# Optimization experiments

Hardware: AMD Instinct MI355X
Metric: run time of the kernel (lower is better)

## Reference

```python
import jax, jax.numpy as jnp
import numpy as np

N, T, CIN = 40000, 32, 8
VW = 64          # back_voxelwise_channels
P = 16           # v2b_maxvoxels (voxels stacked per BEV cell)
BEV_H, BEV_W = 496, 432
EPS = 1e-5


def _bn(key, shape):
    # returns stacked (gamma, beta, running_mean, running_var) along axis -2
    k1, k2, k3 = jax.random.split(key, 3)
    g = 1.0 + 0.1 * jax.random.normal(k1, shape, jnp.float32)
    b = 0.1 * jax.random.normal(k2, shape, jnp.float32)
    m = 0.1 * jax.random.normal(k3, shape, jnp.float32)
    v = jnp.ones(shape, jnp.float32)
    return jnp.stack([g, b, m, v], axis=-2)


def setup_inputs() -> dict:
    key = jax.random.key(0)
    ks = jax.random.split(key, 20)
    features = jax.random.normal(ks[0], (N, T, CIN), jnp.float32)
    cy = jax.random.randint(ks[1], (N, 1), 0, BEV_H)
    cx = jax.random.randint(ks[2], (N, 1), 0, BEV_W)
    coors = jnp.concatenate([cy, cx], axis=1).astype(jnp.int32)
    num_voxels = jax.random.randint(ks[3], (N,), 1, T + 1).astype(jnp.int32)

    def w(k, o, i):
        return jax.random.normal(k, (o, i), jnp.float32) / float(np.sqrt(i))

    return dict(
        features=features, coors=coors, num_voxels=num_voxels,
        vfe1_W=w(ks[4], 8, CIN), vfe1_bn=_bn(ks[5], (8,)),
        vfe2_W=w(ks[6], 32, 16), vfe2_bn=_bn(ks[7], (32,)),
        vfe3_W=w(ks[8], 64, 64), vfe3_bn=_bn(ks[9], (64,)),
        vfe4_W=w(ks[10], 64, 64), vfe4_bn=_bn(ks[11], (64,)),
        bfe1_W=jax.random.normal(ks[12], (16, P, P), jnp.float32) / float(np.sqrt(P)),
        bfe1_bn=_bn(ks[13], (16, P)),
        bfe2_W=jax.random.normal(ks[14], (16, 2, P), jnp.float32) / float(np.sqrt(P)),
        bfe2_bn=_bn(ks[15], (16, 2)),
        bfe3_W=w(ks[16], 128, 128), bfe3_bn=_bn(ks[17], (128,)),
    )


def _forward(features, vfe1_W, vfe1_bn, vfe2_W, vfe2_bn, vfe3_W, vfe3_bn,
             vfe4_W, vfe4_bn, bfe1_W, bfe1_bn, bfe2_W, bfe2_bn, bfe3_W, bfe3_bn,
             coors, num_voxels):
    n, t = features.shape[0], features.shape[1]
    f32 = features.dtype
    mask = (jnp.arange(t)[None, :] < num_voxels[:, None]).astype(f32)[..., None]  # [N,T,1]

    def fe(x, W, bn):  # Linear (no bias) + BatchNorm1d (eval) + Mish
        g, b, m, v = bn
        y = x @ W.T
        y = (y - m) * jax.lax.rsqrt(v + EPS) * g + b
        return y * jnp.tanh(jax.nn.softplus(y))

    def vfe(x, W, bn):  # pointwise FE, max-pool over points, concat
        p = fe(x, W, bn)
        agg = jnp.max(p, axis=1, keepdims=True)
        return jnp.concatenate([p, jnp.broadcast_to(agg, p.shape)], axis=2)

    x1 = vfe(features, vfe1_W, vfe1_bn)           # [N,T,16]
    x2 = vfe(x1, vfe2_W, vfe2_bn) * mask          # [N,T,64]
    x3 = fe(x2, vfe3_W, vfe3_bn)
    x4 = fe(x3, vfe4_W, vfe4_bn) * mask + x2
    voxelwise = jnp.max(x4, axis=1)               # [N,64]

    # ---- voxel2bev: group voxels by BEV cell, stack up to P per cell ----
    cell = coors[:, 0] * BEV_W + coors[:, 1]                         # [N]
    ucell, inv = jnp.unique(cell, return_inverse=True, size=n, fill_value=BEV_H * BEV_W)
    order = jnp.argsort(inv)                                          # stable
    inv_sorted = inv[order]
    pos_sorted = jnp.arange(n) - jnp.searchsorted(inv_sorted, inv_sorted, side='left')
    slot = jnp.zeros(n, jnp.int32).at[order].set(pos_sorted.astype(jnp.int32))
    row = jnp.where(slot < P, inv, n)                                 # overflow -> dropped
    bevs = jnp.zeros((n, P, VW), f32).at[row, jnp.minimum(slot, P - 1)].set(
        voxelwise, mode='drop')                                       # [N,P,64]
    counts = jax.ops.segment_sum(jnp.ones(n, jnp.int32), inv, num_segments=n)
    numv = jnp.minimum(counts, P)
    bevcoors = jnp.stack([ucell // BEV_W, ucell % BEV_W], axis=1)     # [N,2]

    # ---- 16 grouped FE stacks over the slot dimension ----
    x0 = bevs.transpose(0, 2, 1).reshape(n, 16, 4, P)                 # [N,16,4,P]
    m2 = (jnp.arange(P)[None, :] < numv[:, None]).astype(f32)[:, None, None, :]
    y = jnp.einsum('ngip,gqp->ngiq', x0, bfe1_W)                      # [N,16,4,P]
    g1, b1, m1, v1 = (bfe1_bn[None, :, i, None, :] for i in range(4))
    y = (y - m1) * jax.lax.rsqrt(v1 + EPS) * g1 + b1
    y = y * jnp.tanh(jax.nn.softplus(y)) * m2
    z = jnp.einsum('ngip,gcp->ngic', y, bfe2_W)                       # [N,16,4,2]
    g2, b2, m2b, v2 = (bfe2_bn[None, :, i, None, :] for i in range(4))
    z = (z - m2b) * jax.lax.rsqrt(v2 + EPS) * g2 + b2
    z = z * jnp.tanh(jax.nn.softplus(z))
    # torch cat along dim=-1 then view -> layout [N, 4, 16, 2] flattened
    x17 = z.transpose(0, 2, 1, 3).reshape(n, 128)
    x18 = fe(x17, bfe3_W, bfe3_bn)
    x19 = fe(x18, bfe3_W, bfe3_bn)   # original applies bfe3 twice (bfe4 unused)

    bevmap = jnp.zeros((BEV_H, BEV_W, 128), f32).at[
        bevcoors[:, 0], bevcoors[:, 1]].set(x19, mode='drop')
    return bevmap.transpose(2, 1, 0)                                  # [128, W, H]


def reference(features, coors, num_voxels, vfe1_W, vfe1_bn, vfe2_W, vfe2_bn,
              vfe3_W, vfe3_bn, vfe4_W, vfe4_bn, bfe1_W, bfe1_bn, bfe2_W, bfe2_bn,
              bfe3_W, bfe3_bn):
    return _forward(features, vfe1_W, vfe1_bn, vfe2_W, vfe2_bn, vfe3_W, vfe3_bn,
                    vfe4_W, vfe4_bn, bfe1_W, bfe1_bn, bfe2_W, bfe2_bn,
                    bfe3_W, bfe3_bn, coors, num_voxels)
```

## Files before the change

kernel.cpp:

```cpp
#include <hip/hip_runtime.h>

#define BEVW 432
#define BEVH 496
#define NCELL (BEVW*BEVH)
#define NVOX  40000
#define EPSB  1e-5f

typedef float f32x2 __attribute__((ext_vector_type(2)));
typedef float f32x4 __attribute__((ext_vector_type(4)));
typedef unsigned int u32x4 __attribute__((ext_vector_type(4)));
typedef short bf16x8 __attribute__((ext_vector_type(8)));

#define REP8_0(M)  M(0) M(1) M(2) M(3) M(4) M(5) M(6) M(7)
#define REP8_8(M)  M(8) M(9) M(10) M(11) M(12) M(13) M(14) M(15)
#define REP8_16(M) M(16) M(17) M(18) M(19) M(20) M(21) M(22) M(23)
#define REP8_24(M) M(24) M(25) M(26) M(27) M(28) M(29) M(30) M(31)
#define REP16_0(M)  REP8_0(M)  REP8_8(M)
#define REP32_0(M) REP16_0(M) REP8_16(M) REP8_24(M)


__device__ __forceinline__ float mishf(float y) {
    float e = __expf(fminf(y, 40.f));
    float n = e * (e + 2.f);
    return y * n * __builtin_amdgcn_rcpf(n + 2.f);
}

template <int CTRL>
__device__ __forceinline__ float dppmaxf(float a) {
    int p = __builtin_amdgcn_update_dpp(0, __float_as_int(a), CTRL, 0xF, 0xF, true);
    return fmaxf(a, __int_as_float(p));
}
#define WMAX32(a) { \
    a = dppmaxf<0xB1>(a); \
    a = dppmaxf<0x4E>(a); \
    a = dppmaxf<0x141>(a); \
    a = dppmaxf<0x140>(a); \
    a = fmaxf(a, __int_as_float(__builtin_amdgcn_ds_swizzle(__float_as_int(a), 0x401F))); }

__device__ __forceinline__ bf16x8 mkbf8(uint a, uint b, uint c, uint d) {
    u32x4 t = {a, b, c, d};
    return __builtin_bit_cast(bf16x8, t);
}

__device__ __forceinline__ uint splitbf(float x) {
    uint rh = __float_as_uint(x) & 0xFFFF0000u;
    float lof = x - __uint_as_float(rh);
    uint ul = __float_as_uint(lof);
    uint rl = (ul + 0x7FFFu + ((ul >> 16) & 1u)) >> 16;
    return (rh >> 16) | (rl << 16);
}

__global__ __launch_bounds__(256) void setup_kernel(
    const float* __restrict__ vbn1, const float* __restrict__ vbn2,
    const float* __restrict__ vbn3, const float* __restrict__ vbn4,
    const float* __restrict__ bbn1, const float* __restrict__ bbn2,
    const float* __restrict__ bbn3, const float* __restrict__ W4,
    const float* __restrict__ W3g,
    float* __restrict__ fold, ushort* __restrict__ w4fh, ushort* __restrict__ w4fl,
    ushort* __restrict__ w3fh, ushort* __restrict__ w3fl)
{
    int tid = threadIdx.x;
    if (tid < 8)  { float s = vbn1[tid]/sqrtf(vbn1[24+tid]+EPSB);  fold[tid]      = s; fold[8+tid]   = vbn1[8+tid]  - vbn1[16+tid]*s; }
    if (tid < 32) { float s = vbn2[tid]/sqrtf(vbn2[96+tid]+EPSB);  fold[16+tid]   = s; fold[48+tid]  = vbn2[32+tid] - vbn2[64+tid]*s; }
    if (tid < 64) { float s = vbn3[tid]/sqrtf(vbn3[192+tid]+EPSB); fold[80+tid]   = s; fold[144+tid] = vbn3[64+tid] - vbn3[128+tid]*s; }
    if (tid < 64) { float s = vbn4[tid]/sqrtf(vbn4[192+tid]+EPSB); fold[208+tid]  = s; fold[272+tid] = vbn4[64+tid] - vbn4[128+tid]*s; }
    if (tid < 128){ float s = bbn3[tid]/sqrtf(bbn3[384+tid]+EPSB); fold[336+tid]  = s; fold[464+tid] = bbn3[128+tid]- bbn3[256+tid]*s; }
    { int g = tid >> 4, q = tid & 15;
      const float* b = bbn1 + g*64;
      float s = b[q]/sqrtf(b[48+q]+EPSB);
      fold[592+tid] = s; fold[848+tid] = b[16+q] - b[32+q]*s; }
    if (tid < 32) { int g = tid >> 1, c = tid & 1;
      const float* b = bbn2 + g*8;
      float s = b[c]/sqrtf(b[6+c]+EPSB);
      fold[1104+tid] = s; fold[1136+tid] = b[2+c] - b[4+c]*s; }

    for (int i = tid; i < 4096; i += 256) {
        int j = i & 7, ln = (i >> 3) & 63, nt = (i >> 9) & 3, kc = i >> 11;
        int n = (ln & 15) + nt*16;
        int k = kc*32 + (ln >> 4)*8 + j;
        {
            float val = W4[n*64 + k];
            uint rh = __float_as_uint(val) & 0xFFFF0000u;
            float lof = val - __uint_as_float(rh);
            uint ul = __float_as_uint(lof);
            uint rl = (ul + 0x7FFFu + ((ul >> 16) & 1u)) >> 16;
            w4fh[i] = (ushort)(rh >> 16);
            w4fl[i] = (ushort)rl;
        }
        {
            float val = W3g[n*64 + k];
            uint rh = __float_as_uint(val) & 0xFFFF0000u;
            float lof = val - __uint_as_float(rh);
            uint ul = __float_as_uint(lof);
            uint rl = (ul + 0x7FFFu + ((ul >> 16) & 1u)) >> 16;
            w3fh[i] = (ushort)(rh >> 16);
            w3fl[i] = (ushort)rl;
        }
    }
}

#define PAIRS(M) M(0,0,1) M(1,2,3) M(2,4,5) M(3,6,7) M(4,8,9) M(5,10,11) \
  M(6,12,13) M(7,14,15) M(8,16,17) M(9,18,19) M(10,20,21) M(11,22,23) \
  M(12,24,25) M(13,26,27) M(14,28,29) M(15,30,31)

#define MF3(D, AH, AL, BH, BL) \
    D = __builtin_amdgcn_mfma_f32_16x16x32_bf16(AL, BH, D, 0, 0, 0); \
    D = __builtin_amdgcn_mfma_f32_16x16x32_bf16(AH, BL, D, 0, 0, 0); \
    D = __builtin_amdgcn_mfma_f32_16x16x32_bf16(AH, BH, D, 0, 0, 0);

#define DOMTX(SRCP, BHP, BLP, mt, D0, D1, D2, D3) { \
    const uint* ap_ = (SRCP) + ((lane & 15) + 16*(mt))*33 + quad*8; \
    uint u0 = ap_[0], u1 = ap_[1], u2 = ap_[2], u3 = ap_[3]; \
    uint u4 = ap_[4], u5 = ap_[5], u6 = ap_[6], u7 = ap_[7]; \
    bf16x8 Ah = mkbf8(__builtin_amdgcn_perm(u1,u0,0x05040100), __builtin_amdgcn_perm(u3,u2,0x05040100), \
                      __builtin_amdgcn_perm(u5,u4,0x05040100), __builtin_amdgcn_perm(u7,u6,0x05040100)); \
    bf16x8 Al = mkbf8(__builtin_amdgcn_perm(u1,u0,0x07060302), __builtin_amdgcn_perm(u3,u2,0x07060302), \
                      __builtin_amdgcn_perm(u5,u4,0x07060302), __builtin_amdgcn_perm(u7,u6,0x07060302)); \
    { uint4 h = (BHP)[0];   uint4 l = (BLP)[0];   bf16x8 Bh = mkbf8(h.x,h.y,h.z,h.w), Bl = mkbf8(l.x,l.y,l.z,l.w); MF3(D0, Ah, Al, Bh, Bl) } \
    { uint4 h = (BHP)[64];  uint4 l = (BLP)[64];  bf16x8 Bh = mkbf8(h.x,h.y,h.z,h.w), Bl = mkbf8(l.x,l.y,l.z,l.w); MF3(D1, Ah, Al, Bh, Bl) } \
    { uint4 h = (BHP)[128]; uint4 l = (BLP)[128]; bf16x8 Bh = mkbf8(h.x,h.y,h.z,h.w), Bl = mkbf8(l.x,l.y,l.z,l.w); MF3(D2, Ah, Al, Bh, Bl) } \
    { uint4 h = (BHP)[192]; uint4 l = (BLP)[192]; bf16x8 Bh = mkbf8(h.x,h.y,h.z,h.w), Bl = mkbf8(l.x,l.y,l.z,l.w); MF3(D3, Ah, Al, Bh, Bl) } }

__global__ __launch_bounds__(64, 3) void vfe_kernel(
    const float* __restrict__ feat, const int* __restrict__ coors,
    const int* __restrict__ nvx,
    const float* __restrict__ W1, const float* __restrict__ W2,
    const ushort* __restrict__ w3fh, const ushort* __restrict__ w3fl,
    const ushort* __restrict__ w4fh, const ushort* __restrict__ w4fl,
    const float* __restrict__ fold,
    float* __restrict__ voxelwise, int* __restrict__ cnt,
    int* __restrict__ list, int* __restrict__ nact, int* __restrict__ act)
{
    __shared__ char ldsbuf[17152];
    int tid = threadIdx.x;
    int lane = tid;
    int quad = lane >> 4;
    int v = blockIdx.x * 2 + (tid >> 5);
    int vA = blockIdx.x * 2;
    int t = tid & 31;
    uint*  x2s  = (uint*)ldsbuf;
    float* aggL = (float*)(ldsbuf + 16896);

    const float* fp = feat + (v*32 + t)*8;
    float4 fa = *(const float4*)fp;
    float4 fb = *(const float4*)(fp+4);
    int numv = nvx[v];
    float maskf = (t < numv) ? 1.f : 0.f;

#define D1(o) float x1_##o; float m1_##o;
    REP8_0(D1)
#undef D1
#define FE1(o) { const float* w = W1 + (o)*8; \
    float ya = fa.x*w[0] + fa.y*w[1]; float yb = fa.z*w[2] + fa.w*w[3]; \
    float yc = fb.x*w[4] + fb.y*w[5]; float yd = fb.z*w[6] + fb.w*w[7]; \
    float yy = ((ya+yb)+(yc+yd)) * fold[(o)] + fold[8+(o)]; \
    x1_##o = mishf(yy); }
    REP8_0(FE1)
#undef FE1
#define P1(o) { float a = x1_##o; WMAX32(a); m1_##o = a; }
    REP8_0(P1)
#undef P1

    f32x2 x1p_0 = {x1_0,x1_1}, x1p_1 = {x1_2,x1_3}, x1p_2 = {x1_4,x1_5}, x1p_3 = {x1_6,x1_7};
    f32x2 m1p_0 = {m1_0,m1_1}, m1p_1 = {m1_2,m1_3}, m1p_2 = {m1_4,m1_5}, m1p_3 = {m1_6,m1_7};

#define D2(o) float x2_##o; float agg_##o;
    REP32_0(D2)
#undef D2
#define FE2(o) { const f32x2* wp = (const f32x2*)(W2 + (o)*16); \
    f32x2 sa = x1p_0*wp[0]; sa += x1p_1*wp[1]; \
    f32x2 sb = x1p_2*wp[2]; sb += x1p_3*wp[3]; \
    f32x2 sc = m1p_0*wp[4]; sc += m1p_1*wp[5]; \
    f32x2 sd = m1p_2*wp[6]; sd += m1p_3*wp[7]; \
    sa += sb; sc += sd; sa += sc; \
    float yy = (sa.x + sa.y) * fold[16+(o)] + fold[48+(o)]; \
    x2_##o = mishf(yy); }
    REP32_0(FE2)
#undef FE2
#define P2(o) { float a = x2_##o; WMAX32(a); agg_##o = a; }
    REP32_0(P2)
#undef P2

#define PX(i,a,b) f32x2 x2p_##i = {x2_##a, x2_##b}; f32x2 aggp_##i = {agg_##a, agg_##b};
    PAIRS(PX)
#undef PX

    f32x2 maskp = {maskf, maskf};
#define MSK(i) x2p_##i *= maskp; aggp_##i *= maskp;
    REP16_0(MSK)
#undef MSK

    if (t == 0) {
        float* ag = aggL + (lane >> 5)*32;
#define AGW(i) ag[2*(i)] = aggp_##i.x; ag[2*(i)+1] = aggp_##i.y;
        REP16_0(AGW)
#undef AGW
    }

    int nA = __shfl(numv, 0);
    int nB = __shfl(numv, 32);

#define X2W(i) { \
    x2s[lane*33 + 2*(i)]          = splitbf(x2p_##i.x); \
    x2s[lane*33 + 2*(i)+1]        = splitbf(x2p_##i.y); \
    x2s[2112 + lane*33 + 2*(i)]   = splitbf(aggp_##i.x); \
    x2s[2112 + lane*33 + 2*(i)+1] = splitbf(aggp_##i.y); }
    REP16_0(X2W)
#undef X2W

#define E_DECL(i) f32x4 e_##i = {0.f,0.f,0.f,0.f};
    REP16_0(E_DECL)
#undef E_DECL
    {
        const uint4* bh3 = (const uint4*)w3fh + lane;
        const uint4* bl3 = (const uint4*)w3fl + lane;
        DOMTX(x2s, bh3, bl3, 0, e_0, e_1, e_2, e_3)
        DOMTX(x2s, bh3, bl3, 1, e_4, e_5, e_6, e_7)
        DOMTX(x2s, bh3, bl3, 2, e_8, e_9, e_10, e_11)
        DOMTX(x2s, bh3, bl3, 3, e_12, e_13, e_14, e_15)
    }
    {
        const uint4* bh3 = (const uint4*)w3fh + 256 + lane;
        const uint4* bl3 = (const uint4*)w3fl + 256 + lane;
        const uint* sp = x2s + 2112;
        DOMTX(sp, bh3, bl3, 0, e_0, e_1, e_2, e_3)
        DOMTX(sp, bh3, bl3, 1, e_4, e_5, e_6, e_7)
        DOMTX(sp, bh3, bl3, 2, e_8, e_9, e_10, e_11)
        DOMTX(sp, bh3, bl3, 3, e_12, e_13, e_14, e_15)
    }

    int c0 = lane & 15;
    uint* x3st = x2s + 2112;
#define DD(i) f32x4 d_##i = {0.f,0.f,0.f,0.f};
    REP16_0(DD)
#undef DD

#define POST(TI, mt, nt) { \
    float s_ = fold[80 + c0 + 16*(nt)], tb_ = fold[144 + c0 + 16*(nt)]; \
    int col_ = c0 + 16*((nt)&1); \
    int rowb_ = quad*4 + 16*(mt); \
    x3st[(rowb_+0)*33 + col_] = splitbf(mishf(e_##TI.x * s_ + tb_)); \
    x3st[(rowb_+1)*33 + col_] = splitbf(mishf(e_##TI.y * s_ + tb_)); \
    x3st[(rowb_+2)*33 + col_] = splitbf(mishf(e_##TI.z * s_ + tb_)); \
    x3st[(rowb_+3)*33 + col_] = splitbf(mishf(e_##TI.w * s_ + tb_)); }

    {
        POST(0,0,0)  POST(1,0,1)
        POST(4,1,0)  POST(5,1,1)
        POST(8,2,0)  POST(9,2,1)
        POST(12,3,0) POST(13,3,1)
        const uint4* bh4 = (const uint4*)w4fh + lane;
        const uint4* bl4 = (const uint4*)w4fl + lane;
        DOMTX(x3st, bh4, bl4, 0, d_0, d_1, d_2, d_3)
        DOMTX(x3st, bh4, bl4, 1, d_4, d_5, d_6, d_7)
        DOMTX(x3st, bh4, bl4, 2, d_8, d_9, d_10, d_11)
        DOMTX(x3st, bh4, bl4, 3, d_12, d_13, d_14, d_15)
    }
    {
        POST(2,0,2)  POST(3,0,3)
        POST(6,1,2)  POST(7,1,3)
        POST(10,2,2) POST(11,2,3)
        POST(14,3,2) POST(15,3,3)
        const uint4* bh4 = (const uint4*)w4fh + 256 + lane;
        const uint4* bl4 = (const uint4*)w4fl + 256 + lane;
        DOMTX(x3st, bh4, bl4, 0, d_0, d_1, d_2, d_3)
        DOMTX(x3st, bh4, bl4, 1, d_4, d_5, d_6, d_7)
        DOMTX(x3st, bh4, bl4, 2, d_8, d_9, d_10, d_11)
        DOMTX(x3st, bh4, bl4, 3, d_12, d_13, d_14, d_15)
    }
#undef POST

    float s0f = fold[208+c0],    t0f = fold[272+c0];
    float s1f = fold[208+16+c0], t1f = fold[272+16+c0];
    float s2f = fold[208+32+c0], t2f = fold[272+32+c0];
    float s3f = fold[208+48+c0], t3f = fold[272+48+c0];
    float rA2 = aggL[c0],      rA3 = aggL[16+c0];
    float rB2 = aggL[32+c0],   rB3 = aggL[48+c0];
    float pA0=-3.4e38f, pA1=-3.4e38f, pA2=-3.4e38f, pA3=-3.4e38f;
    float pB0=-3.4e38f, pB1=-3.4e38f, pB2=-3.4e38f, pB3=-3.4e38f;

#define RECON(u) (__uint_as_float((u)<<16) + __uint_as_float((u) & 0xFFFF0000u))
#define FTP(D, mt, nt, SS, TT, PV) { \
    int nv = ((mt) >> 1) ? nB : nA; \
    int rf = quad*4 + 16*(mt); \
    int rt = quad*4 + 16*((mt)&1); \
    int cb = c0 + 16*(nt); \
    float m0=(rt+0<nv)?1.f:0.f, m1=(rt+1<nv)?1.f:0.f, m2=(rt+2<nv)?1.f:0.f, m3=(rt+3<nv)?1.f:0.f; \
    uint ua_ = x2s[(rf+0)*33 + cb], ub_ = x2s[(rf+1)*33 + cb]; \
    uint uc_ = x2s[(rf+2)*33 + cb], ud_ = x2s[(rf+3)*33 + cb]; \
    float y0 = mishf(D.x*SS + TT)*m0 + RECON(ua_); \
    float y1 = mishf(D.y*SS + TT)*m1 + RECON(ub_); \
    float y2 = mishf(D.z*SS + TT)*m2 + RECON(uc_); \
    float y3 = mishf(D.w*SS + TT)*m3 + RECON(ud_); \
    PV = fmaxf(PV, fmaxf(fmaxf(y0,y1), fmaxf(y2,y3))); }

#define FTA(D, mt, nt, SS, TT, AG, PV) { \
    int nv = ((mt) >> 1) ? nB : nA; \
    int rt = quad*4 + 16*((mt)&1); \
    float m0=(rt+0<nv)?1.f:0.f, m1=(rt+1<nv)?1.f:0.f, m2=(rt+2<nv)?1.f:0.f, m3=(rt+3<nv)?1.f:0.f; \
    float y0 = (mishf(D.x*SS + TT) + AG)*m0; \
    float y1 = (mishf(D.y*SS + TT) + AG)*m1; \
    float y2 = (mishf(D.z*SS + TT) + AG)*m2; \
    float y3 = (mishf(D.w*SS + TT) + AG)*m3; \
    PV = fmaxf(PV, fmaxf(fmaxf(y0,y1), fmaxf(y2,y3))); }

    FTP(d_0, 0, 0, s0f, t0f, pA0)  FTP(d_1, 0, 1, s1f, t1f, pA1)
    FTA(d_2, 0, 2, s2f, t2f, rA2, pA2)  FTA(d_3, 0, 3, s3f, t3f, rA3, pA3)
    FTP(d_4, 1, 0, s0f, t0f, pA0)  FTP(d_5, 1, 1, s1f, t1f, pA1)
    FTA(d_6, 1, 2, s2f, t2f, rA2, pA2)  FTA(d_7, 1, 3, s3f, t3f, rA3, pA3)
    FTP(d_8, 2, 0, s0f, t0f, pB0)  FTP(d_9, 2, 1, s1f, t1f, pB1)
    FTA(d_10, 2, 2, s2f, t2f, rB2, pB2)  FTA(d_11, 2, 3, s3f, t3f, rB3, pB3)
    FTP(d_12, 3, 0, s0f, t0f, pB0)  FTP(d_13, 3, 1, s1f, t1f, pB1)
    FTA(d_14, 3, 2, s2f, t2f, rB2, pB2)  FTA(d_15, 3, 3, s3f, t3f, rB3, pB3)
#undef FTP
#undef FTA
#undef RECON

#define RED(p) p = fmaxf(p, __shfl_xor(p, 16)); p = fmaxf(p, __shfl_xor(p, 32));
    RED(pA0) RED(pA1) RED(pA2) RED(pA3) RED(pB0) RED(pB1) RED(pB2) RED(pB3)
#undef RED

    if (quad == 0) {
        float* vwA = voxelwise + vA*64;
        vwA[c0] = pA0; vwA[c0+16] = pA1; vwA[c0+32] = pA2; vwA[c0+48] = pA3;
        float* vwB = voxelwise + (vA+1)*64;
        vwB[c0] = pB0; vwB[c0+16] = pB1; vwB[c0+32] = pB2; vwB[c0+48] = pB3;
    }

    if (t == 0) {
        int cell = coors[v*2] * BEVW + coors[v*2+1];
        int pos = atomicAdd(&cnt[cell], 1);
        if (pos < 16) list[cell*16 + pos] = v;
        if (pos == 0) { int k = atomicAdd(nact, 1); act[k] = cell; }
    }
}

__global__ __launch_bounds__(256) void bfe_front(
    const int* __restrict__ nact, const int* __restrict__ act,
    const int* __restrict__ cnt, const int* __restrict__ list,
    const float* __restrict__ voxelwise,
    const float* __restrict__ W1g, const float* __restrict__ W2g,
    const float* __restrict__ fold, float* __restrict__ x17g,
    int* __restrict__ idx)
{
    int n_act = *nact;
    int aidx = blockIdx.x * 4 + (threadIdx.x >> 6);
    if (aidx >= n_act) return;

    int lane = threadIdx.x & 63;
    int g = lane >> 2, ii = lane & 3;
    int cell = act[aidx];
    int numv = min(cnt[cell], 16);
    if (lane == 0) idx[cell] = aidx + 1;

    int myidx = (lane < numv) ? list[cell*16 + lane] : (0x40000000 + lane);
    int rank = 0;
    for (int j = 0; j < numv; j++) { int vj = __shfl(myidx, j); rank += (vj < myidx) ? 1 : 0; }
    if (lane >= numv) rank = lane;
    int sorted = __builtin_amdgcn_ds_permute(rank << 2, myidx);

#define YD(q) float y_##q = 0.f;
    REP16_0(YD)
#undef YD
    for (int p = 0; p < numv; p++) {
        int sv = __shfl(sorted, p);
        float val = voxelwise[sv*64 + lane];
        const float* w = W1g + g*256 + p;
#define BF1(q) y_##q += val * w[(q)*16];
        REP16_0(BF1)
#undef BF1
    }
#define BN1(q) { float yy = y_##q * fold[592 + g*16 + (q)] + fold[848 + g*16 + (q)]; \
    yy = mishf(yy); y_##q = ((q) < numv) ? yy : 0.f; }
    REP16_0(BN1)
#undef BN1

    float z0 = 0.f, z1 = 0.f;
#define BF2(p) z0 += y_##p * W2g[g*32 + (p)]; z1 += y_##p * W2g[g*32 + 16 + (p)];
    REP16_0(BF2)
#undef BF2
    z0 = mishf(z0 * fold[1104 + g*2 + 0] + fold[1136 + g*2 + 0]);
    z1 = mishf(z1 * fold[1104 + g*2 + 1] + fold[1136 + g*2 + 1]);

    int k0 = ii*32 + g*2;
    *(float2*)(x17g + aidx*128 + k0) = make_float2(z0, z1);
}

__global__ __launch_bounds__(512, 4) void bfe3_fused(
    const int* __restrict__ nactp,
    const float* __restrict__ W3, const float* __restrict__ fold,
    float* __restrict__ x17g)
{
    __shared__ float XL[64*128];
    int tid = threadIdx.x;
    int n_act = *nactp;
    int cb = blockIdx.x * 64;

    for (int i = tid; i < 64*32; i += 512) {
        int c = i >> 5, kc = i & 31;
        float4 val = (cb + c < n_act) ? ((const float4*)x17g)[(size_t)(cb+c)*32 + kc]
                                      : make_float4(0.f,0.f,0.f,0.f);
        ((float4*)XL)[c*32 + (kc ^ (c & 31))] = val;
    }
    __syncthreads();

    int wv = __builtin_amdgcn_readfirstlane(tid >> 6);
    int c  = tid & 63;
    int ob = wv * 16;
    int cswz = c & 31;
    const float4* xrow = (const float4*)XL + c*32;
    const float4* W4p = (const float4*)W3;

#define DECLB(q) f32x2 ap_##q = {0.f, 0.f};
#define ACCB(q) { const f32x2* wp_ = (const f32x2*)(W4p + (ob+(q))*32 + kc); \
    ap_##q += xv01 * wp_[0]; ap_##q += xv23 * wp_[1]; }
#define ACTB(q) float a_##q; { float yy = (ap_##q.x + ap_##q.y) * fold[336+ob+(q)] + fold[464+ob+(q)]; a_##q = mishf(yy); }
    {
        REP16_0(DECLB)
        for (int kc = 0; kc < 32; kc++) {
            float4 xv = xrow[kc ^ cswz];
            f32x2 xv01 = {xv.x, xv.y}, xv23 = {xv.z, xv.w};
            REP16_0(ACCB)
        }
        REP16_0(ACTB)
        __syncthreads();
        ((float4*)XL)[c*32 + ((wv*4 + 0) ^ cswz)] = make_float4(a_0,  a_1,  a_2,  a_3);
        ((float4*)XL)[c*32 + ((wv*4 + 1) ^ cswz)] = make_float4(a_4,  a_5,  a_6,  a_7);
        ((float4*)XL)[c*32 + ((wv*4 + 2) ^ cswz)] = make_float4(a_8,  a_9,  a_10, a_11);
        ((float4*)XL)[c*32 + ((wv*4 + 3) ^ cswz)] = make_float4(a_12, a_13, a_14, a_15);
    }
    __syncthreads();

    {
        const float4* yrow = (const float4*)XL + c*32;
        REP16_0(DECLB)
        for (int kc = 0; kc < 32; kc++) {
            float4 xv = yrow[kc ^ cswz];
            f32x2 xv01 = {xv.x, xv.y}, xv23 = {xv.z, xv.w};
            REP16_0(ACCB)
        }
        REP16_0(ACTB)
        float4* dst = (float4*)(x17g + (size_t)(cb + c)*128 + ob);
        dst[0] = make_float4(a_0,  a_1,  a_2,  a_3);
        dst[1] = make_float4(a_4,  a_5,  a_6,  a_7);
        dst[2] = make_float4(a_8,  a_9,  a_10, a_11);
        dst[3] = make_float4(a_12, a_13, a_14, a_15);
    }
#undef DECLB
#undef ACCB
#undef ACTB
}

__global__ __launch_bounds__(512, 2) void bev_write(
    const int* __restrict__ idx, const float* __restrict__ x19c,
    float* __restrict__ out)
{
    __shared__ float XT[128*65];
    int bid = blockIdx.x;
    int cx = bid % BEVW;
    int cy0 = (bid / BEVW) << 6;
    int tid = threadIdx.x;

    int cell_l = tid >> 3;
    int chq = (tid & 7) << 4;
    int cy = cy0 + cell_l;
    float4 v0 = make_float4(0.f,0.f,0.f,0.f), v1 = v0, v2 = v0, v3 = v0;
    if (cy < BEVH) {
        int ai = idx[cy*BEVW + cx] - 1;
        if (ai >= 0) {
            const float4* src = (const float4*)(x19c + (size_t)ai*128 + chq);
            v0 = src[0]; v1 = src[1]; v2 = src[2]; v3 = src[3];
        }
    }
    float* d = XT + chq*65 + cell_l;
    d[0*65]=v0.x;  d[1*65]=v0.y;  d[2*65]=v0.z;  d[3*65]=v0.w;
    d[4*65]=v1.x;  d[5*65]=v1.y;  d[6*65]=v1.z;  d[7*65]=v1.w;
    d[8*65]=v2.x;  d[9*65]=v2.y;  d[10*65]=v2.z; d[11*65]=v2.w;
    d[12*65]=v3.x; d[13*65]=v3.y; d[14*65]=v3.z; d[15*65]=v3.w;
    __syncthreads();

    int wv2 = tid >> 6, lane = tid & 63;
    int cyw = cy0 + lane;
    if (cyw < BEVH) {
        float* op = out + cx*BEVH + cyw;
#pragma unroll
        for (int k = 0; k < 16; k++) {
            int c = (wv2 << 4) + k;
            op[(size_t)c*NCELL] = XT[c*65 + lane];
        }
    }
}

extern "C" void kernel_launch(void* const* d_in, const int* in_sizes, int n_in,
                              void* d_out, int out_size, void* d_ws, size_t ws_size,
                              hipStream_t stream) {
    const float* features = (const float*)d_in[0];
    const int*   coors    = (const int*)d_in[1];
    const int*   num_vox  = (const int*)d_in[2];
    const float* vfe1_W   = (const float*)d_in[3];
    const float* vfe1_bn  = (const float*)d_in[4];
    const float* vfe2_W   = (const float*)d_in[5];
    const float* vfe2_bn  = (const float*)d_in[6];
    const float* vfe3_W   = (const float*)d_in[7];
    const float* vfe3_bn  = (const float*)d_in[8];
    const float* vfe4_W   = (const float*)d_in[9];
    const float* vfe4_bn  = (const float*)d_in[10];
    const float* bfe1_W   = (const float*)d_in[11];
    const float* bfe1_bn  = (const float*)d_in[12];
    const float* bfe2_W   = (const float*)d_in[13];
    const float* bfe2_bn  = (const float*)d_in[14];
    const float* bfe3_W   = (const float*)d_in[15];
    const float* bfe3_bn  = (const float*)d_in[16];
    float* out = (float*)d_out;

    char* ws = (char*)d_ws;
    int*    nact      = (int*)ws;
    int*    cnt       = (int*)(ws + 256);
    int*    idx       = (int*)(ws + 857344);
    int*    list      = (int*)(ws + 1714432);
    float*  voxelwise = (float*)(ws + 15427840);
    int*    act       = (int*)(ws + 25667840);
    float*  x17g      = (float*)(ws + 25827840);
    float*  fold      = (float*)(ws + 46307840);
    ushort* w4fh      = (ushort*)(ws + 46312512);
    ushort* w4fl      = (ushort*)(ws + 46320704);
    ushort* w3fh      = (ushort*)(ws + 46328896);
    ushort* w3fl      = (ushort*)(ws + 46337088);

    (void)hipMemsetAsync(ws, 0, 1714432, stream);

    setup_kernel<<<1, 256, 0, stream>>>(vfe1_bn, vfe2_bn, vfe3_bn, vfe4_bn,
                                        bfe1_bn, bfe2_bn, bfe3_bn, vfe4_W, vfe3_W,
                                        fold, w4fh, w4fl, w3fh, w3fl);
    vfe_kernel<<<NVOX/2, 64, 0, stream>>>(features, coors, num_vox,
                                          vfe1_W, vfe2_W, w3fh, w3fl, w4fh, w4fl, fold,
                                          voxelwise, cnt, list, nact, act);
    bfe_front<<<NVOX/4, 256, 0, stream>>>(nact, act, cnt, list, voxelwise,
                                          bfe1_W, bfe2_W, fold, x17g, idx);
    bfe3_fused<<<(NVOX+63)/64, 512, 0, stream>>>(nact, bfe3_W, fold, x17g);
    bev_write<<<BEVW*8, 512, 0, stream>>>(idx, x17g, out);
}
```

Baseline: 525.3 us.

## Process one voxel per wavefront in vfe_kernel, splitting FE2 channels across half-waves

Changes the VFE kernel from two voxels per 64-lane wave to one voxel per wave. Each half-wave computes 16 of the 32 FE2 output channels for the voxel's 32 points, and the aggregated max is stored in the spare LDS column. This halves per-thread registers and LDS per block and doubles the grid size, with the launch-bounds occupancy hint raised from 3 to 4. In exchange, each MFMA weight fragment is loaded and used for only one voxel, so weight reuse drops and the number of blocks doubles.

Result: slower. 694.9 us (+32.3%).

```diff
diff --git a/kernel.cpp b/kernel.cpp
--- a/kernel.cpp
+++ b/kernel.cpp
@@ -99,9 +99,8 @@
     }
 }
 
-#define PAIRS(M) M(0,0,1) M(1,2,3) M(2,4,5) M(3,6,7) M(4,8,9) M(5,10,11) \
-  M(6,12,13) M(7,14,15) M(8,16,17) M(9,18,19) M(10,20,21) M(11,22,23) \
-  M(12,24,25) M(13,26,27) M(14,28,29) M(15,30,31)
+#define PAIRS8(M) M(0,0,1) M(1,2,3) M(2,4,5) M(3,6,7) M(4,8,9) M(5,10,11) \
+  M(6,12,13) M(7,14,15)
 
 #define MF3(D, AH, AL, BH, BL) \
     D = __builtin_amdgcn_mfma_f32_16x16x32_bf16(AL, BH, D, 0, 0, 0); \
@@ -121,7 +120,7 @@
     { uint4 h = (BHP)[128]; uint4 l = (BLP)[128]; bf16x8 Bh = mkbf8(h.x,h.y,h.z,h.w), Bl = mkbf8(l.x,l.y,l.z,l.w); MF3(D2, Ah, Al, Bh, Bl) } \
     { uint4 h = (BHP)[192]; uint4 l = (BLP)[192]; bf16x8 Bh = mkbf8(h.x,h.y,h.z,h.w), Bl = mkbf8(l.x,l.y,l.z,l.w); MF3(D3, Ah, Al, Bh, Bl) } }
 
-__global__ __launch_bounds__(64, 3) void vfe_kernel(
+__global__ __launch_bounds__(64, 4) void vfe_kernel(
     const float* __restrict__ feat, const int* __restrict__ coors,
     const int* __restrict__ nvx,
     const float* __restrict__ W1, const float* __restrict__ W2,
@@ -131,15 +130,15 @@
     float* __restrict__ voxelwise, int* __restrict__ cnt,
     int* __restrict__ list, int* __restrict__ nact, int* __restrict__ act)
 {
-    __shared__ char ldsbuf[17152];
+    __shared__ char ldsbuf[8448];
     int tid = threadIdx.x;
     int lane = tid;
     int quad = lane >> 4;
-    int v = blockIdx.x * 2 + (tid >> 5);
-    int vA = blockIdx.x * 2;
+    int v = blockIdx.x;
     int t = tid & 31;
-    uint*  x2s  = (uint*)ldsbuf;
-    float* aggL = (float*)(ldsbuf + 16896);
+    int ho = (tid >> 5) << 4;
+    uint*  x2s = (uint*)ldsbuf;
+    float* x2f = (float*)ldsbuf;
 
     const float* fp = feat + (v*32 + t)*8;
     float4 fa = *(const float4*)fp;
@@ -165,74 +164,66 @@
     f32x2 m1p_0 = {m1_0,m1_1}, m1p_1 = {m1_2,m1_3}, m1p_2 = {m1_4,m1_5}, m1p_3 = {m1_6,m1_7};
 
 #define D2(o) float x2_##o; float agg_##o;
-    REP32_0(D2)
+    REP16_0(D2)
 #undef D2
-#define FE2(o) { const f32x2* wp = (const f32x2*)(W2 + (o)*16); \
+#define FE2(o) { const f32x2* wp = (const f32x2*)(W2 + (ho + (o))*16); \
     f32x2 sa = x1p_0*wp[0]; sa += x1p_1*wp[1]; \
     f32x2 sb = x1p_2*wp[2]; sb += x1p_3*wp[3]; \
     f32x2 sc = m1p_0*wp[4]; sc += m1p_1*wp[5]; \
     f32x2 sd = m1p_2*wp[6]; sd += m1p_3*wp[7]; \
     sa += sb; sc += sd; sa += sc; \
-    float yy = (sa.x + sa.y) * fold[16+(o)] + fold[48+(o)]; \
+    float yy = (sa.x + sa.y) * fold[16 + ho + (o)] + fold[48 + ho + (o)]; \
     x2_##o = mishf(yy); }
-    REP32_0(FE2)
+    REP16_0(FE2)
 #undef FE2
 #define P2(o) { float a = x2_##o; WMAX32(a); agg_##o = a; }
-    REP32_0(P2)
+    REP16_0(P2)
 #undef P2
 
 #define PX(i,a,b) f32x2 x2p_##i = {x2_##a, x2_##b}; f32x2 aggp_##i = {agg_##a, agg_##b};
-    PAIRS(PX)
+    PAIRS8(PX)
 #undef PX
 
     f32x2 maskp = {maskf, maskf};
 #define MSK(i) x2p_##i *= maskp; aggp_##i *= maskp;
-    REP16_0(MSK)
+    REP8_0(MSK)
 #undef MSK
 
     if (t == 0) {
-        float* ag = aggL + (lane >> 5)*32;
-#define AGW(i) ag[2*(i)] = aggp_##i.x; ag[2*(i)+1] = aggp_##i.y;
-        REP16_0(AGW)
+#define AGW(i) x2f[(ho + 2*(i))*33 + 32] = aggp_##i.x; x2f[(ho + 2*(i)+1)*33 + 32] = aggp_##i.y;
+        REP8_0(AGW)
 #undef AGW
     }
 
-    int nA = __shfl(numv, 0);
-    int nB = __shfl(numv, 32);
-
 #define X2W(i) { \
-    x2s[lane*33 + 2*(i)]          = splitbf(x2p_##i.x); \
-    x2s[lane*33 + 2*(i)+1]        = splitbf(x2p_##i.y); \
-    x2s[2112 + lane*33 + 2*(i)]   = splitbf(aggp_##i.x); \
-    x2s[2112 + lane*33 + 2*(i)+1] = splitbf(aggp_##i.y); }
-    REP16_0(X2W)
+    x2s[t*33 + ho + 2*(i)]          = splitbf(x2p_##i.x); \
+    x2s[t*33 + ho + 2*(i)+1]        = splitbf(x2p_##i.y); \
+    x2s[1056 + t*33 + ho + 2*(i)]   = splitbf(aggp_##i.x); \
+    x2s[1056 + t*33 + ho + 2*(i)+1] = splitbf(aggp_##i.y); }
+    REP8_0(X2W)
 #undef X2W
 
 #define E_DECL(i) f32x4 e_##i = {0.f,0.f,0.f,0.f};
-    REP16_0(E_DECL)
+    REP8_0(E_DECL)
 #undef E_DECL
     {
         const uint4* bh3 = (const uint4*)w3fh + lane;
         const uint4* bl3 = (const uint4*)w3fl + lane;
         DOMTX(x2s, bh3, bl3, 0, e_0, e_1, e_2, e_3)
         DOMTX(x2s, bh3, bl3, 1, e_4, e_5, e_6, e_7)
-        DOMTX(x2s, bh3, bl3, 2, e_8, e_9, e_10, e_11)
-        DOMTX(x2s, bh3, bl3, 3, e_12, e_13, e_14, e_15)
     }
     {
         const uint4* bh3 = (const uint4*)w3fh + 256 + lane;
         const uint4* bl3 = (const uint4*)w3fl + 256 + lane;
-        const uint* sp = x2s + 2112;
+        const uint* sp = x2s + 1056;
         DOMTX(sp, bh3, bl3, 0, e_0, e_1, e_2, e_3)
         DOMTX(sp, bh3, bl3, 1, e_4, e_5, e_6, e_7)
-        DOMTX(sp, bh3, bl3, 2, e_8, e_9, e_10, e_11)
-        DOMTX(sp, bh3, bl3, 3, e_12, e_13, e_14, e_15)
     }
 
     int c0 = lane & 15;
-    uint* x3st = x2s + 2112;
+    uint* x3st = x2s + 1056;
 #define DD(i) f32x4 d_##i = {0.f,0.f,0.f,0.f};
-    REP16_0(DD)
+    REP8_0(DD)
 #undef DD
 
 #define POST(TI, mt, nt) { \
@@ -247,26 +238,18 @@
     {
         POST(0,0,0)  POST(1,0,1)
         POST(4,1,0)  POST(5,1,1)
-        POST(8,2,0)  POST(9,2,1)
-        POST(12,3,0) POST(13,3,1)
         const uint4* bh4 = (const uint4*)w4fh + lane;
         const uint4* bl4 = (const uint4*)w4fl + lane;
         DOMTX(x3st, bh4, bl4, 0, d_0, d_1, d_2, d_3)
         DOMTX(x3st, bh4, bl4, 1, d_4, d_5, d_6, d_7)
-        DOMTX(x3st, bh4, bl4, 2, d_8, d_9, d_10, d_11)
-        DOMTX(x3st, bh4, bl4, 3, d_12, d_13, d_14, d_15)
     }
     {
         POST(2,0,2)  POST(3,0,3)
         POST(6,1,2)  POST(7,1,3)
-        POST(10,2,2) POST(11,2,3)
-        POST(14,3,2) POST(15,3,3)
         const uint4* bh4 = (const uint4*)w4fh + 256 + lane;
         const uint4* bl4 = (const uint4*)w4fl + 256 + lane;
         DOMTX(x3st, bh4, bl4, 0, d_0, d_1, d_2, d_3)
         DOMTX(x3st, bh4, bl4, 1, d_4, d_5, d_6, d_7)
-        DOMTX(x3st, bh4, bl4, 2, d_8, d_9, d_10, d_11)
-        DOMTX(x3st, bh4, bl4, 3, d_12, d_13, d_14, d_15)
     }
 #undef POST
 
@@ -274,20 +257,16 @@
     float s1f = fold[208+16+c0], t1f = fold[272+16+c0];
     float s2f = fold[208+32+c0], t2f = fold[272+32+c0];
     float s3f = fold[208+48+c0], t3f = fold[272+48+c0];
-    float rA2 = aggL[c0],      rA3 = aggL[16+c0];
-    float rB2 = aggL[32+c0],   rB3 = aggL[48+c0];
-    float pA0=-3.4e38f, pA1=-3.4e38f, pA2=-3.4e38f, pA3=-3.4e38f;
-    float pB0=-3.4e38f, pB1=-3.4e38f, pB2=-3.4e38f, pB3=-3.4e38f;
+    float r2 = x2f[c0*33 + 32], r3 = x2f[(16+c0)*33 + 32];
+    float p0=-3.4e38f, p1=-3.4e38f, p2=-3.4e38f, p3=-3.4e38f;
 
 #define RECON(u) (__uint_as_float((u)<<16) + __uint_as_float((u) & 0xFFFF0000u))
 #define FTP(D, mt, nt, SS, TT, PV) { \
-    int nv = ((mt) >> 1) ? nB : nA; \
-    int rf = quad*4 + 16*(mt); \
-    int rt = quad*4 + 16*((mt)&1); \
+    int rt = quad*4 + 16*(mt); \
     int cb = c0 + 16*(nt); \
-    float m0=(rt+0<nv)?1.f:0.f, m1=(rt+1<nv)?1.f:0.f, m2=(rt+2<nv)?1.f:0.f, m3=(rt+3<nv)?1.f:0.f; \
-    uint ua_ = x2s[(rf+0)*33 + cb], ub_ = x2s[(rf+1)*33 + cb]; \
-    uint uc_ = x2s[(rf+2)*33 + cb], ud_ = x2s[(rf+3)*33 + cb]; \
+    float m0=(rt+0<numv)?1.f:0.f, m1=(rt+1<numv)?1.f:0.f, m2=(rt+2<numv)?1.f:0.f, m3=(rt+3<numv)?1.f:0.f; \
+    uint ua_ = x2s[(rt+0)*33 + cb], ub_ = x2s[(rt+1)*33 + cb]; \
+    uint uc_ = x2s[(rt+2)*33 + cb], ud_ = x2s[(rt+3)*33 + cb]; \
     float y0 = mishf(D.x*SS + TT)*m0 + RECON(ua_); \
     float y1 = mishf(D.y*SS + TT)*m1 + RECON(ub_); \
     float y2 = mishf(D.z*SS + TT)*m2 + RECON(uc_); \
@@ -295,39 +274,32 @@
     PV = fmaxf(PV, fmaxf(fmaxf(y0,y1), fmaxf(y2,y3))); }
 
 #define FTA(D, mt, nt, SS, TT, AG, PV) { \
-    int nv = ((mt) >> 1) ? nB : nA; \
-    int rt = quad*4 + 16*((mt)&1); \
-    float m0=(rt+0<nv)?1.f:0.f, m1=(rt+1<nv)?1.f:0.f, m2=(rt+2<nv)?1.f:0.f, m3=(rt+3<nv)?1.f:0.f; \
+    int rt = quad*4 + 16*(mt); \
+    float m0=(rt+0<numv)?1.f:0.f, m1=(rt+1<numv)?1.f:0.f, m2=(rt+2<numv)?1.f:0.f, m3=(rt+3<numv)?1.f:0.f; \
     float y0 = (mishf(D.x*SS + TT) + AG)*m0; \
     float y1 = (mishf(D.y*SS + TT) + AG)*m1; \
     float y2 = (mishf(D.z*SS + TT) + AG)*m2; \
     float y3 = (mishf(D.w*SS + TT) + AG)*m3; \
     PV = fmaxf(PV, fmaxf(fmaxf(y0,y1), fmaxf(y2,y3))); }
 
-    FTP(d_0, 0, 0, s0f, t0f, pA0)  FTP(d_1, 0, 1, s1f, t1f, pA1)
-    FTA(d_2, 0, 2, s2f, t2f, rA2, pA2)  FTA(d_3, 0, 3, s3f, t3f, rA3, pA3)
-    FTP(d_4, 1, 0, s0f, t0f, pA0)  FTP(d_5, 1, 1, s1f, t1f, pA1)
-    FTA(d_6, 1, 2, s2f, t2f, rA2, pA2)  FTA(d_7, 1, 3, s3f, t3f, rA3, pA3)
-    FTP(d_8, 2, 0, s0f, t0f, pB0)  FTP(d_9, 2, 1, s1f, t1f, pB1)
-    FTA(d_10, 2, 2, s2f, t2f, rB2, pB2)  FTA(d_11, 2, 3, s3f, t3f, rB3, pB3)
-    FTP(d_12, 3, 0, s0f, t0f, pB0)  FTP(d_13, 3, 1, s1f, t1f, pB1)
-    FTA(d_14, 3, 2, s2f, t2f, rB2, pB2)  FTA(d_15, 3, 3, s3f, t3f, rB3, pB3)
+    FTP(d_0, 0, 0, s0f, t0f, p0)  FTP(d_1, 0, 1, s1f, t1f, p1)
+    FTA(d_2, 0, 2, s2f, t2f, r2, p2)  FTA(d_3, 0, 3, s3f, t3f, r3, p3)
+    FTP(d_4, 1, 0, s0f, t0f, p0)  FTP(d_5, 1, 1, s1f, t1f, p1)
+    FTA(d_6, 1, 2, s2f, t2f, r2, p2)  FTA(d_7, 1, 3, s3f, t3f, r3, p3)
 #undef FTP
 #undef FTA
 #undef RECON
 
 #define RED(p) p = fmaxf(p, __shfl_xor(p, 16)); p = fmaxf(p, __shfl_xor(p, 32));
-    RED(pA0) RED(pA1) RED(pA2) RED(pA3) RED(pB0) RED(pB1) RED(pB2) RED(pB3)
+    RED(p0) RED(p1) RED(p2) RED(p3)
 #undef RED
 
     if (quad == 0) {
-        float* vwA = voxelwise + vA*64;
-        vwA[c0] = pA0; vwA[c0+16] = pA1; vwA[c0+32] = pA2; vwA[c0+48] = pA3;
-        float* vwB = voxelwise + (vA+1)*64;
-        vwB[c0] = pB0; vwB[c0+16] = pB1; vwB[c0+32] = pB2; vwB[c0+48] = pB3;
-    }
-
-    if (t == 0) {
+        float* vw = voxelwise + v*64;
+        vw[c0] = p0; vw[c0+16] = p1; vw[c0+32] = p2; vw[c0+48] = p3;
+    }
+
+    if (lane == 0) {
         int cell = coors[v*2] * BEVW + coors[v*2+1];
         int pos = atomicAdd(&cnt[cell], 1);
         if (pos < 16) list[cell*16 + pos] = v;
@@ -532,9 +504,9 @@
     setup_kernel<<<1, 256, 0, stream>>>(vfe1_bn, vfe2_bn, vfe3_bn, vfe4_bn,
                                         bfe1_bn, bfe2_bn, bfe3_bn, vfe4_W, vfe3_W,
                                         fold, w4fh, w4fl, w3fh, w3fl);
-    vfe_kernel<<<NVOX/2, 64, 0, stream>>>(features, coors, num_vox,
-                                          vfe1_W, vfe2_W, w3fh, w3fl, w4fh, w4fl, fold,
-                                          voxelwise, cnt, list, nact, act);
+    vfe_kernel<<<NVOX, 64, 0, stream>>>(features, coors, num_vox,
+                                        vfe1_W, vfe2_W, w3fh, w3fl, w4fh, w4fl, fold,
+                                        voxelwise, cnt, list, nact, act);
     bfe_front<<<NVOX/4, 256, 0, stream>>>(nact, act, cnt, list, voxelwise,
                                           bfe1_W, bfe2_W, fold, x17g, idx);
     bfe3_fused<<<(NVOX+63)/64, 512, 0, stream>>>(nact, bfe3_W, fold, x17g);
```
